# Optimization experiments

Measured on AMD Instinct MI355X. Metric: run time of the kernel, lower is better.

The kernel has to match this reference:

```python
import jax, jax.numpy as jnp
import numpy as np

B, S, HID = 2, 2048, 2048
NH, NKV, HD = 16, 4, 128
GROUPS = NH // NKV
SCALING = HD ** -0.5
ROPE_THETA = 10000.0
NEG_INF = -1e9


def _rope_tables(seq_len, head_dim, batch):
    inv_freq = 1.0 / (ROPE_THETA ** (jnp.arange(0, head_dim, 2, dtype=jnp.float32) / head_dim))
    t = jnp.arange(seq_len, dtype=jnp.float32)
    freqs = jnp.outer(t, inv_freq)                      # [S, HD/2]
    emb = jnp.concatenate([freqs, freqs], axis=-1)      # [S, HD]
    cos = jnp.broadcast_to(jnp.cos(emb)[None], (batch, seq_len, head_dim))
    sin = jnp.broadcast_to(jnp.sin(emb)[None], (batch, seq_len, head_dim))
    return cos, sin


def setup_inputs() -> dict:
    key = jax.random.key(0)
    k1, k2, k3, k4, k5 = jax.random.split(key, 5)
    hidden_states = jax.random.normal(k1, (B, S, HID), dtype=jnp.float32)
    cos, sin = _rope_tables(S, HD, B)
    # HF-style additive causal mask (already includes causality)
    causal = jnp.tril(jnp.ones((S, S), dtype=bool))
    attention_mask = jnp.where(causal, 0.0, NEG_INF).astype(jnp.float32)[None, None]
    attention_mask = jnp.broadcast_to(attention_mask, (B, 1, S, S))
    std = HID ** -0.5
    Wq = jax.random.normal(k2, (HID, NH * HD), dtype=jnp.float32) * std
    Wk = jax.random.normal(k3, (HID, NKV * HD), dtype=jnp.float32) * std
    Wv = jax.random.normal(k4, (HID, NKV * HD), dtype=jnp.float32) * std
    Wo = jax.random.normal(k5, (NH * HD, HID), dtype=jnp.float32) * std
    return {"hidden_states": hidden_states, "cos": cos, "sin": sin,
            "attention_mask": attention_mask, "Wq": Wq, "Wk": Wk, "Wv": Wv, "Wo": Wo}


def _rotate_half(x):
    x1, x2 = jnp.split(x, 2, axis=-1)
    return jnp.concatenate([-x2, x1], axis=-1)


def _apply_rope(q, k, cos, sin):
    # q: [B,NH,S,HD]; k: [B,NKV,S,HD]; cos/sin: [B,S,HD] -> unsqueeze head dim
    cos = cos[:, None]
    sin = sin[:, None]
    q = q * cos + _rotate_half(q) * sin
    k = k * cos + _rotate_half(k) * sin
    return q, k


def reference(hidden_states, cos, sin, attention_mask, Wq, Wk, Wv, Wo):
    b, s, _ = hidden_states.shape
    q = jnp.einsum('bsh,hd->bsd', hidden_states, Wq).reshape(b, s, NH, HD).transpose(0, 2, 1, 3)
    k = jnp.einsum('bsh,hd->bsd', hidden_states, Wk).reshape(b, s, NKV, HD).transpose(0, 2, 1, 3)
    v = jnp.einsum('bsh,hd->bsd', hidden_states, Wv).reshape(b, s, NKV, HD).transpose(0, 2, 1, 3)
    q, k = _apply_rope(q, k, cos, sin)
    # repeat_kv: [B,NKV,S,HD] -> [B,NH,S,HD]
    k = jnp.repeat(k, GROUPS, axis=1)
    v = jnp.repeat(v, GROUPS, axis=1)
    scores = jnp.einsum('bhqd,bhkd->bhqk', q, k) * SCALING
    scores = scores + attention_mask[:, :, :, :s]
    attn_weights = jax.nn.softmax(scores.astype(jnp.float32), axis=-1).astype(q.dtype)
    attn_output = jnp.einsum('bhqk,bhkd->bhqd', attn_weights, v)
    attn_output = attn_output.transpose(0, 2, 1, 3).reshape(b, s, NH * HD)
    attn_output = jnp.einsum('bsd,dh->bsh', attn_output, Wo)
    return attn_output, attn_weights
```

## Files before the change

### kernel.cpp

```cpp
#include <hip/hip_runtime.h>
#include <hip/hip_bf16.h>
#include <math.h>

typedef unsigned short u16;
typedef __bf16 bf16_t;
typedef bf16_t bf16x8 __attribute__((ext_vector_type(8)));
typedef float f32x4 __attribute__((ext_vector_type(4)));
typedef float fvec4 __attribute__((ext_vector_type(4)));

#define DEVI static __device__ __forceinline__

constexpr int BATCH = 2, SEQ = 2048, HIDDEN = 2048, NH = 16, NKV = 4, HD = 128;
constexpr int GROUPS = NH / NKV;
constexpr float SCALE = 0.08838834764831845f;

DEVI u16 f2bf(float x){
  unsigned u = __float_as_uint(x);
  u += 0x7FFFu + ((u >> 16) & 1u);
  return (u16)(u >> 16);
}
DEVI float bf2f(u16 h){ return __uint_as_float(((unsigned)h) << 16); }

DEVI void nt_store4(float* p, float a, float b, float c, float d){
  fvec4 v = {a, b, c, d};
  __builtin_nontemporal_store(v, reinterpret_cast<fvec4*>(p));
}

union FragU { uint4 u; bf16x8 b; };
DEVI bf16x8 ldfrag(const u16* p){
  FragU f; f.u = *reinterpret_cast<const uint4*>(p); return f.b;
}
DEVI f32x4 mfma(bf16x8 a, bf16x8 b, f32x4 c){
  return __builtin_amdgcn_mfma_f32_16x16x32_bf16(a, b, c, 0, 0, 0);
}

DEVI void gll16(const u16* g, u16* lds_base){
  __builtin_amdgcn_global_load_lds(
      (const __attribute__((address_space(1))) unsigned int*)g,
      (__attribute__((address_space(3))) unsigned int*)lds_base, 16, 0, 0);
}

__global__ void k_cvt(const float* __restrict__ in, u16* __restrict__ out, int n8){
  int i = blockIdx.x * blockDim.x + threadIdx.x;
  if (i >= n8) return;
  float4 a = reinterpret_cast<const float4*>(in)[i * 2];
  float4 b = reinterpret_cast<const float4*>(in)[i * 2 + 1];
  ushort4 lo, hi;
  lo.x = f2bf(a.x); lo.y = f2bf(a.y); lo.z = f2bf(a.z); lo.w = f2bf(a.w);
  hi.x = f2bf(b.x); hi.y = f2bf(b.y); hi.z = f2bf(b.z); hi.w = f2bf(b.w);
  reinterpret_cast<ushort4*>(out)[i * 2] = lo;
  reinterpret_cast<ushort4*>(out)[i * 2 + 1] = hi;
}

__global__ void k_wt(const float* __restrict__ W, u16* __restrict__ dst,
                     int K, int N){
  __shared__ float tile[32][33];
  int k0 = blockIdx.x * 32, n0 = blockIdx.y * 32;
  int c = threadIdx.x & 31, r = threadIdx.x >> 5;
#pragma unroll
  for (int rr = 0; rr < 32; rr += 8)
    tile[r + rr][c] = W[(size_t)(k0 + r + rr) * N + n0 + c];
  __syncthreads();
#pragma unroll
  for (int rr = 0; rr < 32; rr += 8)
    dst[(size_t)(n0 + r + rr) * K + k0 + c] = f2bf(tile[c][r + rr]);
}

__global__ __launch_bounds__(256, 2) void k_gemm(
    const u16* __restrict__ Ah, const u16* __restrict__ Bh,
    float* __restrict__ C, int M, int N, int K){
  extern __shared__ u16 smem[];
  u16* sA = smem;
  u16* sB = sA + 4096;
  int tid = threadIdx.x, lane = tid & 63, w = tid >> 6;
  int wm = w >> 1, wn = w & 1;
  int ml = lane & 15, kg = lane >> 4, kl8 = kg * 8;
  int m0 = blockIdx.x * 128, n0 = blockIdx.y * 128;
  int srow = lane >> 2, scol = (lane & 3) * 8;
  f32x4 acc[4][4] = {};
  for (int k0 = 0; k0 < K; k0 += 32){
    __syncthreads();
#pragma unroll
    for (int i = 0; i < 2; ++i){
      int g = i * 4 + w;
      size_t ga = (size_t)(g * 16 + srow) * K + k0 + scol;
      gll16(Ah + (size_t)m0 * K + ga, sA + g * 512);
      gll16(Bh + (size_t)n0 * K + ga, sB + g * 512);
    }
    __syncthreads();
    bf16x8 bh[4];
#pragma unroll
    for (int fn = 0; fn < 4; ++fn)
      bh[fn] = ldfrag(sB + (wn * 64 + fn * 16 + ml) * 32 + kl8);
#pragma unroll
    for (int fm = 0; fm < 4; ++fm){
      bf16x8 ah = ldfrag(sA + (wm * 64 + fm * 16 + ml) * 32 + kl8);
#pragma unroll
      for (int fn = 0; fn < 4; ++fn)
        acc[fm][fn] = mfma(ah, bh[fn], acc[fm][fn]);
    }
  }
  float* cst = (float*)smem;
#pragma unroll
  for (int c = 0; c < 4; ++c){
    __syncthreads();
    if (wm == (c >> 1)){
      int f0 = (c & 1) * 2;
#pragma unroll
      for (int ff = 0; ff < 2; ++ff)
#pragma unroll
        for (int r = 0; r < 4; ++r)
          cst[(ff * 16 + kg * 4 + r) * 130 + wn * 64 + (f0 + ff) * 0 + 0 + wn * 0 +
              (  0)] = 0.f;
    }
    if (wm == (c >> 1)){
      int f0 = (c & 1) * 2;
#pragma unroll
      for (int ff = 0; ff < 2; ++ff){
        int fm = f0 + ff;
#pragma unroll
        for (int fn = 0; fn < 4; ++fn)
#pragma unroll
          for (int r = 0; r < 4; ++r)
            cst[(ff * 16 + kg * 4 + r) * 130 + wn * 64 + fn * 16 + ml] =
                acc[fm][fn][r];
      }
    }
    __syncthreads();
#pragma unroll
    for (int ps = 0; ps < 4; ++ps){
      int rowc = ps * 8 + (tid >> 5);
      int cc = (tid & 31) * 4;
      float4 v = *reinterpret_cast<const float4*>(cst + rowc * 130 + cc);
      *reinterpret_cast<float4*>(C + (size_t)(m0 + c * 32 + rowc) * N + n0 + cc) = v;
    }
  }
}

__global__ void k_rope(const float* __restrict__ src, const float* __restrict__ cosb,
                       const float* __restrict__ sinb, u16* __restrict__ dhi,
                       int nheads){
  int row = blockIdx.x * 4 + (threadIdx.x >> 6);
  int d = threadIdx.x & 63;
  int h = row % nheads;
  int bs = row / nheads;
  int s = bs & (SEQ - 1);
  int b = bs >> 11;
  const float* sp = src + (size_t)row * HD;
  float x1 = sp[d], x2 = sp[d + 64];
  size_t ci = ((size_t)b * SEQ + s) * HD;
  float o1 = x1 * cosb[ci + d] - x2 * sinb[ci + d];
  float o2 = x2 * cosb[ci + d + 64] + x1 * sinb[ci + d + 64];
  size_t di = (((size_t)b * nheads + h) * SEQ + s) * HD;
  dhi[di + d] = f2bf(o1);
  dhi[di + d + 64] = f2bf(o2);
}

__global__ void k_vt(const float* __restrict__ src, u16* __restrict__ dst){
  __shared__ float tile[32][33];
  int b = blockIdx.z >> 2, kv = blockIdx.z & 3;
  int s0 = blockIdx.x * 32, d0 = blockIdx.y * 32;
  int c = threadIdx.x & 31, r = threadIdx.x >> 5;
#pragma unroll
  for (int rr = 0; rr < 32; rr += 8)
    tile[r + rr][c] = src[(((size_t)b * SEQ + s0 + r + rr) * NKV + kv) * HD + d0 + c];
  __syncthreads();
#pragma unroll
  for (int rr = 0; rr < 32; rr += 8)
    dst[(((size_t)b * NKV + kv) * HD + d0 + r + rr) * SEQ + s0 + c] = f2bf(tile[c][r + rr]);
}

__global__ __launch_bounds__(256, 3) void k_stat(
    const u16* __restrict__ qh, const u16* __restrict__ kh,
    float* __restrict__ pm, float* __restrict__ pl){
  int x = blockIdx.x;
  int qt = (int)((sqrtf(8.f * (float)x + 1.f) - 1.f) * 0.5f);
  while (qt * (qt + 1) / 2 > x) --qt;
  while ((qt + 1) * (qt + 2) / 2 <= x) ++qt;
  int kt = x - qt * (qt + 1) / 2;
  int h = blockIdx.y, b = blockIdx.z;
  int tid = threadIdx.x, lane = tid & 63, w = tid >> 6;
  int wm = w >> 1, wn = w & 1;
  int ml = lane & 15, kg = lane >> 4;
  const u16* qbh = qh + ((size_t)b * NH + h) * SEQ * HD;
  const u16* kbh = kh + ((size_t)b * NKV + h / GROUPS) * SEQ * HD;

  f32x4 acc[4][4] = {};
#pragma unroll
  for (int ds = 0; ds < 4; ++ds){
    int kk = ds * 32 + kg * 8;
    bf16x8 bh[4], ah[4];
#pragma unroll
    for (int fn = 0; fn < 4; ++fn)
      bh[fn] = ldfrag(kbh + (size_t)(kt * 128 + wn * 64 + fn * 16 + ml) * HD + kk);
#pragma unroll
    for (int fm = 0; fm < 4; ++fm)
      ah[fm] = ldfrag(qbh + (size_t)(qt * 128 + wm * 64 + fm * 16 + ml) * HD + kk);
#pragma unroll
    for (int fm = 0; fm < 4; ++fm)
#pragma unroll
      for (int fn = 0; fn < 4; ++fn)
        acc[fm][fn] = mfma(ah[fm], bh[fn], acc[fm][fn]);
  }
  bool diag = (kt == qt);
  __shared__ float sm[2][128], sl[2][128];
#pragma unroll
  for (int fm = 0; fm < 4; ++fm){
#pragma unroll
    for (int r = 0; r < 4; ++r){
      int lr = wm * 64 + fm * 16 + kg * 4 + r;
      int rg = qt * 128 + lr;
      float sv[4];
#pragma unroll
      for (int fn = 0; fn < 4; ++fn){
        float s = acc[fm][fn][r] * SCALE;
        int cg = kt * 128 + wn * 64 + fn * 16 + ml;
        sv[fn] = (diag && cg > rg) ? -1e30f : s;
      }
      float tm = fmaxf(fmaxf(sv[0], sv[1]), fmaxf(sv[2], sv[3]));
#pragma unroll
      for (int xm = 1; xm < 16; xm <<= 1) tm = fmaxf(tm, __shfl_xor(tm, xm, 64));
      float ps = 0.f;
#pragma unroll
      for (int fn = 0; fn < 4; ++fn)
        ps += (sv[fn] < -1e29f) ? 0.f : __expf(sv[fn] - tm);
#pragma unroll
      for (int xm = 1; xm < 16; xm <<= 1) ps += __shfl_xor(ps, xm, 64);
      if (ml == 0){ sm[wn][lr] = tm; sl[wn][lr] = ps; }
    }
  }
  __syncthreads();
  if (tid < 128){
    float m0 = sm[0][tid], m1 = sm[1][tid];
    float mm = fmaxf(m0, m1);
    float e0 = (m0 < -1e29f) ? 0.f : __expf(m0 - mm);
    float e1 = (m1 < -1e29f) ? 0.f : __expf(m1 - mm);
    float ll = sl[0][tid] * e0 + sl[1][tid] * e1;
    size_t pidx = ((((size_t)b * NH + h) * 16 + qt) * 16 + kt) * 128 + tid;
    pm[pidx] = mm;
    pl[pidx] = ll;
  }
}

__global__ void k_mlred(const float* __restrict__ pm, const float* __restrict__ pl,
                        float* __restrict__ mrow, float* __restrict__ lrinv){
  int idx = blockIdx.x * blockDim.x + threadIdx.x;
  int row = idx & (SEQ - 1);
  int bh = idx >> 11;
  int qt = row >> 7, rt = row & 127;
  size_t base = (((size_t)bh * 16 + qt) * 16) * 128 + rt;
  float m = -1e30f;
  for (int kt = 0; kt <= qt; ++kt) m = fmaxf(m, pm[base + (size_t)kt * 128]);
  float l = 0.f;
  for (int kt = 0; kt <= qt; ++kt)
    l += pl[base + (size_t)kt * 128] * __expf(pm[base + (size_t)kt * 128] - m);
  mrow[(size_t)bh * SEQ + row] = m;
  lrinv[(size_t)bh * SEQ + row] = 1.0f / l;
}

__global__ __launch_bounds__(256, 2) void k_fuse2(
    const u16* __restrict__ qh, const u16* __restrict__ kh,
    const u16* __restrict__ vt, const float* __restrict__ mrow,
    const float* __restrict__ lrinv, float* __restrict__ wmat,
    u16* __restrict__ ao){
  int p = blockIdx.x, h = blockIdx.y, b = blockIdx.z;
  int tid = threadIdx.x, lane = tid & 63, w = tid >> 6;
  int rh = w >> 1, dh = w & 1;
  int ml = lane & 15, kg = lane >> 4;
  const u16* qb = qh + ((size_t)b * NH + h) * SEQ * HD;
  const u16* kb = kh + ((size_t)b * NKV + h / GROUPS) * SEQ * HD;
  const u16* vb = vt + ((size_t)b * NKV + h / GROUPS) * HD * SEQ;
  float* wout = wmat + ((size_t)b * NH + h) * SEQ * SEQ;
  const float* mr = mrow + (size_t)(b * NH + h) * SEQ;
  const float* lr = lrinv + (size_t)(b * NH + h) * SEQ;

  __shared__ char smem[34816];
  u16* plds = (u16*)smem;
  float* olds = (float*)(smem + 18432);
  u16* obuf = (u16*)smem;

  int kext_s[2];

  for (int half = 0; half < 2; ++half){
    int i = half ? (63 - p) : p;
    int r0 = i * 32;
    int kext = ((r0 + 32 + 127) >> 7) << 7;
    kext_s[half] = kext;

    bf16x8 qf[4];
#pragma unroll
    for (int ds = 0; ds < 4; ++ds)
      qf[ds] = ldfrag(qb + (size_t)(r0 + rh * 16 + ml) * HD + ds * 32 + kg * 8);

    float mv[4], rlv[4];
#pragma unroll
    for (int r = 0; r < 4; ++r){
      int rg = r0 + rh * 16 + kg * 4 + r;
      mv[r] = mr[rg];
      rlv[r] = lr[rg];
    }

    u16* myp0 = plds + (size_t)w * 1152;
    u16* myp1 = plds + 4608 + (size_t)w * 1152;
    auto store_prev = [&](int c0p, u16* buf){
#pragma unroll
      for (int pass = 0; pass < 4; ++pass){
        int row = pass * 4 + (lane >> 4);
        int cc = (lane & 15) * 4;
        uint2 uv = *reinterpret_cast<const uint2*>(buf + row * 72 + cc);
        nt_store4(wout + (size_t)(r0 + rh * 16 + row) * SEQ + c0p + dh * 64 + cc,
                  bf2f((u16)(uv.x & 0xFFFF)), bf2f((u16)(uv.x >> 16)),
                  bf2f((u16)(uv.y & 0xFFFF)), bf2f((u16)(uv.y >> 16)));
      }
    };

    f32x4 oacc[8] = {};
    int nb = kext >> 7;
    for (int g = 0; g < nb; ++g){
      int c0 = g << 7;
      u16* cur = (g & 1) ? myp1 : myp0;
      u16* prv = (g & 1) ? myp0 : myp1;
#pragma unroll
      for (int s = 0; s < 2; ++s){
        int cb = c0 + dh * 64 + s * 32;
        bf16x8 kf[4][2];
#pragma unroll
        for (int ds = 0; ds < 4; ++ds)
#pragma unroll
          for (int j = 0; j < 2; ++j)
            kf[ds][j] = ldfrag(kb + (size_t)(cb + j * 16 + ml) * HD + ds * 32 + kg * 8);
        bf16x8 vf[8];
#pragma unroll
        for (int vfn = 0; vfn < 8; ++vfn)
          vf[vfn] = ldfrag(vb + (size_t)(vfn * 16 + ml) * SEQ + cb + kg * 8);
        asm volatile("" ::: "memory");
        if (s == 0 && g > 0) store_prev(c0 - 128, prv);
        f32x4 sacc[2] = {};
#pragma unroll
        for (int ds = 0; ds < 4; ++ds)
#pragma unroll
          for (int j = 0; j < 2; ++j)
            sacc[j] = mfma(qf[ds], kf[ds][j], sacc[j]);
#pragma unroll
        for (int j = 0; j < 2; ++j)
#pragma unroll
          for (int r = 0; r < 4; ++r){
            int rg = r0 + rh * 16 + kg * 4 + r;
            int cg = cb + j * 16 + ml;
            float sv = sacc[j][r] * SCALE;
            float wv = (cg <= rg) ? __expf(sv - mv[r]) * rlv[r] : 0.f;
            cur[(kg * 4 + r) * 72 + s * 32 + j * 16 + ml] = f2bf(wv);
          }
        bf16x8 pf = ldfrag(cur + ml * 72 + s * 32 + kg * 8);
#pragma unroll
        for (int vfn = 0; vfn < 8; ++vfn)
          oacc[vfn] = mfma(pf, vf[vfn], oacc[vfn]);
      }
    }
    store_prev(kext - 128, (nb & 1) ? myp0 : myp1);

    if (dh == 1){
#pragma unroll
      for (int vfn = 0; vfn < 8; ++vfn)
#pragma unroll
        for (int r = 0; r < 4; ++r)
          olds[((size_t)rh * 16 + kg * 4 + r) * 128 + vfn * 16 + ml] = oacc[vfn][r];
    }
    __syncthreads();
    if (dh == 0){
#pragma unroll
      for (int vfn = 0; vfn < 8; ++vfn)
#pragma unroll
        for (int r = 0; r < 4; ++r){
          float sum = oacc[vfn][r] +
                      olds[((size_t)rh * 16 + kg * 4 + r) * 128 + vfn * 16 + ml];
          obuf[(rh * 16 + kg * 4 + r) * 136 + vfn * 16 + ml] = f2bf(sum);
        }
    }
    __syncthreads();
#pragma unroll
    for (int pass = 0; pass < 2; ++pass){
      int row = pass * 16 + (tid >> 4);
      int cc = (tid & 15) * 8;
      uint4 a = *reinterpret_cast<const uint4*>(obuf + row * 136 + cc);
      *reinterpret_cast<uint4*>(ao + ((size_t)b * SEQ + r0 + row) * (NH * HD) +
                                h * HD + cc) = a;
    }
    __syncthreads();
  }

#pragma unroll
  for (int half = 0; half < 2; ++half){
    int i = half ? (63 - p) : p;
    int r0 = i * 32;
    int kext = kext_s[half];
    for (int rr = tid >> 5; rr < 32; rr += 8)
      for (int c = kext + (tid & 31) * 4; c < SEQ; c += 128)
        nt_store4(wout + (size_t)(r0 + rr) * SEQ + c, 0.f, 0.f, 0.f, 0.f);
  }
}

extern "C" void kernel_launch(void* const* d_in, const int* in_sizes, int n_in,
                              void* d_out, int out_size, void* d_ws, size_t ws_size,
                              hipStream_t stream){
  (void)in_sizes; (void)n_in; (void)out_size; (void)ws_size;
  const float* hs   = (const float*)d_in[0];
  const float* cosb = (const float*)d_in[1];
  const float* sinb = (const float*)d_in[2];
  const float* Wq = (const float*)d_in[4];
  const float* Wk = (const float*)d_in[5];
  const float* Wv = (const float*)d_in[6];
  const float* Wo = (const float*)d_in[7];
  float* out  = (float*)d_out;
  float* wmat = out + (size_t)BATCH * SEQ * HIDDEN;

  char* ws = (char*)d_ws;
  size_t off = 0;
  auto alloc = [&](size_t bytes)->char*{
    char* p = ws + off; off += (bytes + 255) & ~(size_t)255; return p;
  };
  u16* hs_b  = (u16*)alloc(16777216);
  u16* wq_t  = (u16*)alloc(8388608);
  u16* wk_t  = (u16*)alloc(2097152);
  u16* wv_t  = (u16*)alloc(2097152);
  u16* wo_t  = (u16*)alloc(8388608);
  float* Qraw = (float*)alloc(33554432);
  float* Kraw = (float*)alloc(8388608);
  float* Vraw = (float*)alloc(8388608);
  u16* q_hi = (u16*)alloc(16777216);
  u16* k_hi = (u16*)alloc(4194304);
  u16* v_t  = (u16*)alloc(4194304);
  float* mrow = (float*)alloc(262144);
  float* lrow = (float*)alloc(262144);
  float* pm   = (float*)alloc(4194304);
  float* pl   = (float*)alloc(4194304);
  u16* ao = (u16*)Qraw;

  size_t lds_gemm = 17408;

  k_cvt<<<4096, 256, 0, stream>>>(hs, hs_b, BATCH * SEQ * HIDDEN / 8);
  k_wt<<<dim3(64, 64), 256, 0, stream>>>(Wq, wq_t, HIDDEN, NH * HD);
  k_wt<<<dim3(64, 16), 256, 0, stream>>>(Wk, wk_t, HIDDEN, NKV * HD);
  k_wt<<<dim3(64, 16), 256, 0, stream>>>(Wv, wv_t, HIDDEN, NKV * HD);
  k_wt<<<dim3(64, 64), 256, 0, stream>>>(Wo, wo_t, NH * HD, HIDDEN);

  k_gemm<<<dim3(32, 16), 256, lds_gemm, stream>>>(hs_b, wq_t, Qraw, 4096, 2048, 2048);
  k_gemm<<<dim3(32,  4), 256, lds_gemm, stream>>>(hs_b, wk_t, Kraw, 4096,  512, 2048);
  k_gemm<<<dim3(32,  4), 256, lds_gemm, stream>>>(hs_b, wv_t, Vraw, 4096,  512, 2048);

  k_rope<<<BATCH * SEQ * NH  / 4, 256, 0, stream>>>(Qraw, cosb, sinb, q_hi, NH);
  k_rope<<<BATCH * SEQ * NKV / 4, 256, 0, stream>>>(Kraw, cosb, sinb, k_hi, NKV);
  k_stat<<<dim3(136, 16, 2), 256, 0, stream>>>(q_hi, k_hi, pm, pl);
  k_vt<<<dim3(64, 4, 8), 256, 0, stream>>>(Vraw, v_t);
  k_mlred<<<256, 256, 0, stream>>>(pm, pl, mrow, lrow);

  k_fuse2<<<dim3(32, 16, 2), 256, 0, stream>>>(q_hi, k_hi, v_t, mrow, lrow,
                                               wmat, (u16*)ao);

  k_gemm<<<dim3(32, 16), 256, lds_gemm, stream>>>(ao, wo_t, out, 4096, 2048, 2048);
}
```

Before: 592.4 us.

## Fuse RoPE and bf16 head-major store into Q/K projection GEMM epilogue

Adds a GEMM variant whose epilogue applies rotary embedding from the staged fp32 tile in LDS and writes bf16 head-major Q/K directly. This removes the separate RoPE kernels and the fp32 Qraw/Kraw round trip through global memory. It also drops a redundant zero-store loop in the GEMM epilogue and gives the attention output its own buffer. The epilogue does more work: it reads cos/sin from global memory and uses branchy per-half math.

New measurement: 581.1 us. No clear change (-1.9%).

```diff
diff --git a/kernel.cpp b/kernel.cpp
--- a/kernel.cpp
+++ b/kernel.cpp
@@ -107,15 +107,6 @@
     if (wm == (c >> 1)){
       int f0 = (c & 1) * 2;
 #pragma unroll
-      for (int ff = 0; ff < 2; ++ff)
-#pragma unroll
-        for (int r = 0; r < 4; ++r)
-          cst[(ff * 16 + kg * 4 + r) * 130 + wn * 64 + (f0 + ff) * 0 + 0 + wn * 0 +
-              (  0)] = 0.f;
-    }
-    if (wm == (c >> 1)){
-      int f0 = (c & 1) * 2;
-#pragma unroll
       for (int ff = 0; ff < 2; ++ff){
         int fm = f0 + ff;
 #pragma unroll
@@ -137,23 +128,86 @@
   }
 }
 
-__global__ void k_rope(const float* __restrict__ src, const float* __restrict__ cosb,
-                       const float* __restrict__ sinb, u16* __restrict__ dhi,
-                       int nheads){
-  int row = blockIdx.x * 4 + (threadIdx.x >> 6);
-  int d = threadIdx.x & 63;
-  int h = row % nheads;
-  int bs = row / nheads;
-  int s = bs & (SEQ - 1);
-  int b = bs >> 11;
-  const float* sp = src + (size_t)row * HD;
-  float x1 = sp[d], x2 = sp[d + 64];
-  size_t ci = ((size_t)b * SEQ + s) * HD;
-  float o1 = x1 * cosb[ci + d] - x2 * sinb[ci + d];
-  float o2 = x2 * cosb[ci + d + 64] + x1 * sinb[ci + d + 64];
-  size_t di = (((size_t)b * nheads + h) * SEQ + s) * HD;
-  dhi[di + d] = f2bf(o1);
-  dhi[di + d + 64] = f2bf(o2);
+__global__ __launch_bounds__(256, 2) void k_gemmr(
+    const u16* __restrict__ Ah, const u16* __restrict__ Bh,
+    const float* __restrict__ cosb, const float* __restrict__ sinb,
+    u16* __restrict__ dst, int nheads, int K){
+  extern __shared__ u16 smem[];
+  u16* sA = smem;
+  u16* sB = sA + 4096;
+  int tid = threadIdx.x, lane = tid & 63, w = tid >> 6;
+  int wm = w >> 1, wn = w & 1;
+  int ml = lane & 15, kg = lane >> 4, kl8 = kg * 8;
+  int m0 = blockIdx.x * 128, h = blockIdx.y;
+  int n0 = h * 128;
+  int srow = lane >> 2, scol = (lane & 3) * 8;
+  f32x4 acc[4][4] = {};
+  for (int k0 = 0; k0 < K; k0 += 32){
+    __syncthreads();
+#pragma unroll
+    for (int i = 0; i < 2; ++i){
+      int g = i * 4 + w;
+      size_t ga = (size_t)(g * 16 + srow) * K + k0 + scol;
+      gll16(Ah + (size_t)m0 * K + ga, sA + g * 512);
+      gll16(Bh + (size_t)n0 * K + ga, sB + g * 512);
+    }
+    __syncthreads();
+    bf16x8 bh[4];
+#pragma unroll
+    for (int fn = 0; fn < 4; ++fn)
+      bh[fn] = ldfrag(sB + (wn * 64 + fn * 16 + ml) * 32 + kl8);
+#pragma unroll
+    for (int fm = 0; fm < 4; ++fm){
+      bf16x8 ah = ldfrag(sA + (wm * 64 + fm * 16 + ml) * 32 + kl8);
+#pragma unroll
+      for (int fn = 0; fn < 4; ++fn)
+        acc[fm][fn] = mfma(ah, bh[fn], acc[fm][fn]);
+    }
+  }
+  float* cst = (float*)smem;
+#pragma unroll
+  for (int c = 0; c < 4; ++c){
+    __syncthreads();
+    if (wm == (c >> 1)){
+      int f0 = (c & 1) * 2;
+#pragma unroll
+      for (int ff = 0; ff < 2; ++ff){
+        int fm = f0 + ff;
+#pragma unroll
+        for (int fn = 0; fn < 4; ++fn)
+#pragma unroll
+          for (int r = 0; r < 4; ++r)
+            cst[(ff * 16 + kg * 4 + r) * 130 + wn * 64 + fn * 16 + ml] =
+                acc[fm][fn][r];
+      }
+    }
+    __syncthreads();
+#pragma unroll
+    for (int ps = 0; ps < 4; ++ps){
+      int rowc = ps * 8 + (tid >> 5);
+      int cc = (tid & 31) * 4;
+      int gr = m0 + c * 32 + rowc;
+      int bb = gr >> 11, s = gr & (SEQ - 1);
+      size_t ci = ((size_t)bb * SEQ + s) * HD + cc;
+      float4 vv = *reinterpret_cast<const float4*>(cst + rowc * 130 + cc);
+      float4 pv = *reinterpret_cast<const float4*>(
+          cst + rowc * 130 + (cc < 64 ? cc + 64 : cc - 64));
+      float4 cs = *reinterpret_cast<const float4*>(cosb + ci);
+      float4 sn = *reinterpret_cast<const float4*>(sinb + ci);
+      float o0, o1, o2, o3;
+      if (cc < 64){
+        o0 = vv.x * cs.x - pv.x * sn.x; o1 = vv.y * cs.y - pv.y * sn.y;
+        o2 = vv.z * cs.z - pv.z * sn.z; o3 = vv.w * cs.w - pv.w * sn.w;
+      } else {
+        o0 = vv.x * cs.x + pv.x * sn.x; o1 = vv.y * cs.y + pv.y * sn.y;
+        o2 = vv.z * cs.z + pv.z * sn.z; o3 = vv.w * cs.w + pv.w * sn.w;
+      }
+      ushort4 ov;
+      ov.x = f2bf(o0); ov.y = f2bf(o1); ov.z = f2bf(o2); ov.w = f2bf(o3);
+      *reinterpret_cast<ushort4*>(
+          dst + (((size_t)bb * nheads + h) * SEQ + s) * HD + cc) = ov;
+    }
+  }
 }
 
 __global__ void k_vt(const float* __restrict__ src, u16* __restrict__ dst){
@@ -424,17 +478,15 @@
   u16* wk_t  = (u16*)alloc(2097152);
   u16* wv_t  = (u16*)alloc(2097152);
   u16* wo_t  = (u16*)alloc(8388608);
-  float* Qraw = (float*)alloc(33554432);
-  float* Kraw = (float*)alloc(8388608);
   float* Vraw = (float*)alloc(8388608);
   u16* q_hi = (u16*)alloc(16777216);
   u16* k_hi = (u16*)alloc(4194304);
   u16* v_t  = (u16*)alloc(4194304);
+  u16* ao   = (u16*)alloc(16777216);
   float* mrow = (float*)alloc(262144);
   float* lrow = (float*)alloc(262144);
   float* pm   = (float*)alloc(4194304);
   float* pl   = (float*)alloc(4194304);
-  u16* ao = (u16*)Qraw;
 
   size_t lds_gemm = 17408;
 
@@ -444,12 +496,10 @@
   k_wt<<<dim3(64, 16), 256, 0, stream>>>(Wv, wv_t, HIDDEN, NKV * HD);
   k_wt<<<dim3(64, 64), 256, 0, stream>>>(Wo, wo_t, NH * HD, HIDDEN);
 
-  k_gemm<<<dim3(32, 16), 256, lds_gemm, stream>>>(hs_b, wq_t, Qraw, 4096, 2048, 2048);
-  k_gemm<<<dim3(32,  4), 256, lds_gemm, stream>>>(hs_b, wk_t, Kraw, 4096,  512, 2048);
-  k_gemm<<<dim3(32,  4), 256, lds_gemm, stream>>>(hs_b, wv_t, Vraw, 4096,  512, 2048);
-
-  k_rope<<<BATCH * SEQ * NH  / 4, 256, 0, stream>>>(Qraw, cosb, sinb, q_hi, NH);
-  k_rope<<<BATCH * SEQ * NKV / 4, 256, 0, stream>>>(Kraw, cosb, sinb, k_hi, NKV);
+  k_gemmr<<<dim3(32, 16), 256, lds_gemm, stream>>>(hs_b, wq_t, cosb, sinb, q_hi, NH, 2048);
+  k_gemmr<<<dim3(32,  4), 256, lds_gemm, stream>>>(hs_b, wk_t, cosb, sinb, k_hi, NKV, 2048);
+  k_gemm<<<dim3(32,  4), 256, lds_gemm, stream>>>(hs_b, wv_t, Vraw, 4096, 512, 2048);
+
   k_stat<<<dim3(136, 16, 2), 256, 0, stream>>>(q_hi, k_hi, pm, pl);
   k_vt<<<dim3(64, 4, 8), 256, 0, stream>>>(Vraw, v_t);
   k_mlred<<<256, 256, 0, stream>>>(pm, pl, mrow, lrow);
```
